# Kernel tuning notes

Hardware: AMD Instinct MI355X
Metric: run time of the kernel (lower is better)

## Reference

```python
import jax, jax.numpy as jnp
import numpy as np

B, N, D = 2, 8192, 1024
H, Dh = 16, 64
P = H * Dh
EPS = 1e-6
DECAY_BIAS_SHIFT = 2.0


def setup_inputs() -> dict:
    key = jax.random.key(0)
    ks = jax.random.split(key, 7)
    s_in = 1.0 / np.sqrt(D)
    s_out = 1.0 / np.sqrt(P)
    return {
        "x": jax.random.normal(ks[0], (B, N, D), jnp.float32),
        "Wq": jax.random.normal(ks[1], (D, P), jnp.float32) * s_in,
        "Wk": jax.random.normal(ks[2], (D, P), jnp.float32) * s_in,
        "Wv": jax.random.normal(ks[3], (D, P), jnp.float32) * s_in,
        "Wo": jax.random.normal(ks[4], (P, D), jnp.float32) * s_out,
        "Wa": jax.random.normal(ks[5], (D, H), jnp.float32) * s_in,
        "ba": jnp.zeros((H,), jnp.float32),
    }


def _elu_plus_one(x):
    return jax.nn.elu(x) + 1.0


def _ssd_scan(q, k, v, a, eps):
    # q,k,v: (B,H,N,Dh); a: (B,H,N) in (0,1)
    # Recurrence: S_t = a_t*S_{t-1} + k_t v_t^T ; z_t = a_t*z_{t-1} + k_t
    # out_t = (q_t @ S_t) / (q_t . z_t + eps)
    qT = jnp.moveaxis(q, 2, 0)  # (N,B,H,Dh)
    kT = jnp.moveaxis(k, 2, 0)
    vT = jnp.moveaxis(v, 2, 0)
    aT = jnp.moveaxis(a, 2, 0)  # (N,B,H)

    Bb, Hh, _, Dk = q.shape
    Dv = v.shape[-1]
    S0 = jnp.zeros((Bb, Hh, Dk, Dv), q.dtype)
    z0 = jnp.zeros((Bb, Hh, Dk), q.dtype)

    def step(carry, inp):
        S, z = carry
        qt, kt, vt, at = inp
        S = at[..., None, None] * S + kt[..., :, None] * vt[..., None, :]
        z = at[..., None] * z + kt
        num = jnp.einsum("bhk,bhkv->bhv", qt, S)
        den = jnp.einsum("bhk,bhk->bh", qt, z) + eps
        return (S, z), num / den[..., None]

    _, outT = jax.lax.scan(step, (S0, z0), (qT, kT, vT, aT))
    return jnp.moveaxis(outT, 0, 2)  # (B,H,N,Dv)


def reference(x, Wq, Wk, Wv, Wo, Wa, ba):
    b, n, _ = x.shape
    q = (x @ Wq).reshape(b, n, H, Dh).transpose(0, 2, 1, 3)
    k = (x @ Wk).reshape(b, n, H, Dh).transpose(0, 2, 1, 3)
    v = (x @ Wv).reshape(b, n, H, Dh).transpose(0, 2, 1, 3)
    q = _elu_plus_one(q)
    k = _elu_plus_one(k)
    a = jax.nn.sigmoid(x @ Wa + ba + DECAY_BIAS_SHIFT)  # (B,N,H)
    a = a.transpose(0, 2, 1)  # (B,H,N)
    out = _ssd_scan(q, k, v, a, EPS)  # (B,H,N,Dh)
    out = out.transpose(0, 2, 1, 3).reshape(b, n, P)
    return out @ Wo
```

## Files before the change

kernel.cpp:

```cpp
#include <hip/hip_runtime.h>
#include <stdint.h>

#define HH 16
#define DH 64
#define DD 1024
#define PP 1024
#define NNLEN 8192
#define BBATCH 2
#define MM (BBATCH*NNLEN)
#define CCHUNK 128
#define LCH 64
#define NGRP 16
#define GCH 8
#define EPSV 1e-6f

typedef unsigned short u16;
typedef __attribute__((ext_vector_type(4))) unsigned short u16x4;
typedef __attribute__((ext_vector_type(8))) unsigned short u16x8;
typedef __attribute__((ext_vector_type(8))) __bf16 bf16x8;
typedef __attribute__((ext_vector_type(4))) float f32x4;

__device__ __forceinline__ u16 f2bf(float f) {
  unsigned x = __float_as_uint(f);
  return (u16)((x + 0x7fffu + ((x >> 16) & 1u)) >> 16);
}
__device__ __forceinline__ float bf2f(u16 u) {
  return __uint_as_float(((unsigned)u) << 16);
}

__device__ __forceinline__ void gl2lds16(const void* g, void* l) {
  __builtin_amdgcn_global_load_lds(
      reinterpret_cast<__attribute__((address_space(1))) void*>(
          reinterpret_cast<uintptr_t>(g)),
      reinterpret_cast<__attribute__((address_space(3))) void*>(
          reinterpret_cast<uintptr_t>(l)),
      16, 0, 0);
}

__device__ __forceinline__ bf16x8 ldsw(const u16* base, int row, int col) {
  union { u16x8 u; bf16x8 b; } cv;
  cv.u = *(const u16x8*)&base[row * 64 + (col ^ ((row & 7) << 3))];
  return cv.b;
}

__global__ __launch_bounds__(256)
void prep_all(const float* __restrict__ x, u16* __restrict__ xb,
              const float* __restrict__ Wq, u16* __restrict__ WqT,
              const float* __restrict__ Wk, u16* __restrict__ WkT,
              const float* __restrict__ Wv, u16* __restrict__ WvT,
              const float* __restrict__ Wo, u16* __restrict__ WoT,
              const float* __restrict__ Wa, u16* __restrict__ WaT) {
  __shared__ float tile[32][33];
  const int bid = blockIdx.x;
  const int tid = threadIdx.x;
  if (bid < 8192) {
    size_t i = ((size_t)bid * 256 + tid) * 8;
    f32x4 a = *(const f32x4*)(x + i);
    f32x4 b = *(const f32x4*)(x + i + 4);
    u16x8 o;
    o[0] = f2bf(a[0]); o[1] = f2bf(a[1]); o[2] = f2bf(a[2]); o[3] = f2bf(a[3]);
    o[4] = f2bf(b[0]); o[5] = f2bf(b[1]); o[6] = f2bf(b[2]); o[7] = f2bf(b[3]);
    *(u16x8*)(xb + i) = o;
    return;
  }
  if (bid < 12288) {
    const int t = (bid - 8192) >> 10;
    const int sub = (bid - 8192) & 1023;
    const float* in = (t == 0) ? Wq : (t == 1) ? Wk : (t == 2) ? Wv : Wo;
    u16* out = (t == 0) ? WqT : (t == 1) ? WkT : (t == 2) ? WvT : WoT;
    const int bx = (sub & 31) * 32, by = (sub >> 5) * 32;
    const int tx = tid & 31, ty = tid >> 5;
    for (int i2 = ty; i2 < 32; i2 += 8)
      tile[i2][tx] = in[(size_t)(by + i2) * 1024 + bx + tx];
    __syncthreads();
    for (int i2 = ty; i2 < 32; i2 += 8)
      out[(size_t)(bx + i2) * 1024 + by + tx] = f2bf(tile[tx][i2]);
    return;
  }
  {
    int idx = (bid - 12288) * 256 + tid;
    WaT[idx] = f2bf(Wa[(idx & 1023) * 16 + (idx >> 10)]);
  }
}

__global__ __launch_bounds__(256)
void a_proj(const u16* __restrict__ xb, const u16* __restrict__ WaT,
            const float* __restrict__ ba, float* __restrict__ abuf) {
  __shared__ __align__(16) u16 As[256 * 32];
  __shared__ __align__(16) u16 Bs[16 * 32];
  const int tid = threadIdx.x;
  const int brow = blockIdx.x * 256;
  const int l = tid & 63, wid = tid >> 6;
  const int la = l & 15, kb8 = (l >> 4) * 8;
  const int sr = tid >> 2, se = (tid & 3) * 8;

  f32x4 acc[4];
#pragma unroll
  for (int mi = 0; mi < 4; ++mi) acc[mi] = (f32x4){0.f, 0.f, 0.f, 0.f};

  for (int kt = 0; kt < 32; ++kt) {
    const int k0 = kt * 32;
    __syncthreads();
#pragma unroll
    for (int i = 0; i < 4; ++i)
      gl2lds16(xb + (size_t)(brow + i * 64 + sr) * DD + k0 + se,
               &As[i * 2048 + wid * 512]);
    if (wid == 0)
      gl2lds16(WaT + (size_t)(l >> 2) * DD + k0 + (l & 3) * 8, &Bs[0]);
    __syncthreads();
    union { u16x8 u; bf16x8 b; } cvb;
    cvb.u = *(const u16x8*)&Bs[la * 32 + kb8];
#pragma unroll
    for (int mi = 0; mi < 4; ++mi) {
      union { u16x8 u; bf16x8 b; } cva;
      cva.u = *(const u16x8*)&As[(wid * 64 + mi * 16 + la) * 32 + kb8];
      acc[mi] = __builtin_amdgcn_mfma_f32_16x16x32_bf16(cva.b, cvb.b, acc[mi], 0, 0, 0);
    }
  }
  const float bav = ba[la];
#pragma unroll
  for (int mi = 0; mi < 4; ++mi)
#pragma unroll
    for (int rr = 0; rr < 4; ++rr) {
      int row = brow + wid * 64 + mi * 16 + ((l >> 4) << 2) + rr;
      float t = acc[mi][rr] + bav + 2.0f;
      abuf[(size_t)row * HH + la] = 1.f / (1.f + __expf(-t));
    }
}

template<int NCT, int ROUTE>
__global__ __launch_bounds__(512)
void gemm_db(const u16* __restrict__ A, const u16* __restrict__ Bt,
             void* __restrict__ Cout) {
  __shared__ __align__(16) u16 As[2][256 * 64];
  __shared__ __align__(16) u16 Bs[2][256 * 64];
  const int tid = threadIdx.x;
  const int nwg = gridDim.x;
  const int f = blockIdx.x;
  const int swz = (f & 7) * (nwg >> 3) + (f >> 3);
  const int brow = (swz / NCT) * 256;
  const int bcol = (swz % NCT) * 256;
  const int l = tid & 63;
  const int wid = tid >> 6;
  const int wr = wid >> 2;
  const int wc = wid & 3;
  const int la = l & 15, kb8 = (l >> 4) * 8;
  const int K = 1024;
  const int srow = l >> 3;
  const int scol = ((l & 7) * 8) ^ (srow << 3);
  const int ldso = (wid * 2) * 512;

  f32x4 acc[8][4];
#pragma unroll
  for (int i = 0; i < 8; ++i)
#pragma unroll
    for (int j = 0; j < 4; ++j) acc[i][j] = (f32x4){0.f, 0.f, 0.f, 0.f};

#pragma unroll
  for (int h = 0; h < 2; ++h)
#pragma unroll
    for (int j = 0; j < 2; ++j) {
      const int r0 = h * 128 + (wid * 2 + j) * 8 + srow;
      gl2lds16(A  + (size_t)(brow + r0) * K + scol, &As[0][h * 8192 + ldso + j * 512]);
      gl2lds16(Bt + (size_t)(bcol + r0) * K + scol, &Bs[0][h * 8192 + ldso + j * 512]);
    }
  asm volatile("s_waitcnt vmcnt(0)" ::: "memory");
  __builtin_amdgcn_s_barrier();

  const int NKT = K / 64;
  for (int kt = 0; kt < NKT; ++kt) {
    const u16* lA = As[kt & 1];
    const u16* lB = Bs[kt & 1];
    u16* nA = As[(kt + 1) & 1];
    u16* nB = Bs[(kt + 1) & 1];
    const int knext = (kt + 1) * 64;
    const bool more = (kt + 1 < NKT);

    if (more) {
#pragma unroll
      for (int h = 0; h < 2; ++h)
#pragma unroll
        for (int j = 0; j < 2; ++j) {
          const int r0 = h * 128 + (wid * 2 + j) * 8 + srow;
          gl2lds16(A  + (size_t)(brow + r0) * K + knext + scol,
                   nA + h * 8192 + ldso + j * 512);
          gl2lds16(Bt + (size_t)(bcol + r0) * K + knext + scol,
                   nB + h * 8192 + ldso + j * 512);
        }
    }

    bf16x8 af[4][2], bfr[4][2];
#pragma unroll
    for (int m2 = 0; m2 < 4; ++m2)
#pragma unroll
      for (int kk = 0; kk < 2; ++kk)
        af[m2][kk] = ldsw(lA, wr * 128 + m2 * 16 + la, kk * 32 + kb8);
#pragma unroll
    for (int n2 = 0; n2 < 4; ++n2)
#pragma unroll
      for (int kk = 0; kk < 2; ++kk)
        bfr[n2][kk] = ldsw(lB, wc * 64 + n2 * 16 + la, kk * 32 + kb8);

    __builtin_amdgcn_s_setprio(1);
#pragma unroll
    for (int m2 = 0; m2 < 4; ++m2)
#pragma unroll
      for (int n2 = 0; n2 < 4; ++n2)
#pragma unroll
        for (int kk = 0; kk < 2; ++kk)
          acc[m2][n2] = __builtin_amdgcn_mfma_f32_16x16x32_bf16(
              af[m2][kk], bfr[n2][kk], acc[m2][n2], 0, 0, 0);
    __builtin_amdgcn_s_setprio(0);

#pragma unroll
    for (int m2 = 0; m2 < 4; ++m2)
#pragma unroll
      for (int kk = 0; kk < 2; ++kk)
        af[m2][kk] = ldsw(lA, wr * 128 + 64 + m2 * 16 + la, kk * 32 + kb8);

    __builtin_amdgcn_s_setprio(1);
#pragma unroll
    for (int m2 = 0; m2 < 4; ++m2)
#pragma unroll
      for (int n2 = 0; n2 < 4; ++n2)
#pragma unroll
        for (int kk = 0; kk < 2; ++kk)
          acc[4 + m2][n2] = __builtin_amdgcn_mfma_f32_16x16x32_bf16(
              af[m2][kk], bfr[n2][kk], acc[4 + m2][n2], 0, 0, 0);
    __builtin_amdgcn_s_setprio(0);

    if (more) {
      asm volatile("s_waitcnt vmcnt(0)" ::: "memory");
      __builtin_amdgcn_s_barrier();
    }
  }

  const int wrow = wr * 128, wcol = wc * 64;
  if (ROUTE) {
    u16* base = (u16*)Cout + (size_t)(bcol >> 10) * ((size_t)MM * 1024);
    const bool act = (bcol < 2048);
#pragma unroll
    for (int mi = 0; mi < 8; ++mi)
#pragma unroll
      for (int ni = 0; ni < 4; ++ni)
#pragma unroll
        for (int rr = 0; rr < 4; ++rr) {
          int row = brow + wrow + mi * 16 + ((l >> 4) << 2) + rr;
          int c2 = (bcol & 1023) + wcol + ni * 16 + la;
          float v = acc[mi][ni][rr];
          if (act) v = v > 0.f ? v + 1.f : __expf(v);
          base[(size_t)row * 1024 + c2] = f2bf(v);
        }
  } else {
#pragma unroll
    for (int mi = 0; mi < 8; ++mi)
#pragma unroll
      for (int ni = 0; ni < 4; ++ni)
#pragma unroll
        for (int rr = 0; rr < 4; ++rr) {
          int row = brow + wrow + mi * 16 + ((l >> 4) << 2) + rr;
          int col = bcol + wcol + ni * 16 + la;
          ((float*)Cout)[(size_t)row * 1024 + col] = acc[mi][ni][rr];
        }
  }
}

__global__ __launch_bounds__(256)
void chunk_local_scan(const u16* __restrict__ kb, const u16* __restrict__ vb,
                      const float* __restrict__ abuf,
                      u16* __restrict__ Sbuf, float* __restrict__ zbuf,
                      float* __restrict__ cAbuf,
                      float* __restrict__ GAgg, float* __restrict__ zGAgg,
                      float* __restrict__ dpbuf) {
  const int g = blockIdx.x & (NGRP - 1);
  const int bh = blockIdx.x >> 4;
  const int h = bh & (HH - 1);
  const int b = bh >> 4;
  __shared__ __align__(16) u16 KT[64 * 64];
  __shared__ __align__(16) u16 VTl[64 * 64];
  __shared__ float wsh[64];
  __shared__ float dchs;
  const int tid = threadIdx.x;
  const int r = tid >> 2, e = (tid & 3) * 16;
  const int l = tid & 63, w = tid >> 6;
  const int kb8 = (l >> 4) << 3, la = l & 15;
  const int dw = 16 * w + ((l >> 4) << 2);
  const int dkz = tid >> 2, tqz = (tid & 3) * 16, swkz = (dkz & 7) << 3;

  f32x4 run[4];
#pragma unroll
  for (int ni = 0; ni < 4; ++ni) run[ni] = (f32x4){0.f, 0.f, 0.f, 0.f};
  float zrun = 0.f;
  float rp = 1.f;

  for (int i = 0; i < GCH; ++i) {
    const int c = g * GCH + i;
    const int blkc = bh * CCHUNK + c;
    const int rowbase = b * NNLEN + c * LCH;

    const u16* kp = kb + (size_t)(rowbase + r) * PP + h * DH + e;
    const u16* vp = vb + (size_t)(rowbase + r) * PP + h * DH + e;
    u16x8 k0 = *(const u16x8*)kp, k1 = *(const u16x8*)(kp + 8);
    u16x8 v0 = *(const u16x8*)vp, v1 = *(const u16x8*)(vp + 8);

    if (tid < 64) {
      float v = __logf(abuf[(size_t)(rowbase + tid) * HH + h]);
#pragma unroll
      for (int d = 1; d < 64; d <<= 1) {
        float u = __shfl_up(v, d);
        if (tid >= d) v += u;
      }
      cAbuf[(size_t)blkc * 64 + tid] = v;
      float tot = __shfl(v, 63);
      wsh[tid] = __expf(tot - v);
      if (tid == 0) dchs = __expf(tot);
    }
    __syncthreads();

    {
      const float wt = wsh[r];
#pragma unroll
      for (int j = 0; j < 8; ++j) {
        int d0 = e + j, d1 = e + 8 + j;
        KT[d0 * 64 + (r ^ ((d0 & 7) << 3))] = f2bf(bf2f(k0[j]) * wt);
        KT[d1 * 64 + (r ^ ((d1 & 7) << 3))] = f2bf(bf2f(k1[j]) * wt);
        VTl[d0 * 64 + (r ^ ((d0 & 7) << 3))] = v0[j];
        VTl[d1 * 64 + (r ^ ((d1 & 7) << 3))] = v1[j];
      }
    }
    __syncthreads();
    const float dch = dchs;

    f32x4 s[4];
#pragma unroll
    for (int ni = 0; ni < 4; ++ni) s[ni] = (f32x4){0.f, 0.f, 0.f, 0.f};
#pragma unroll
    for (int kk = 0; kk < 2; ++kk) {
      bf16x8 av = ldsw(VTl, 16 * w + la, kk * 32 + kb8);
#pragma unroll
      for (int ni = 0; ni < 4; ++ni)
        s[ni] = __builtin_amdgcn_mfma_f32_16x16x32_bf16(
            av, ldsw(KT, 16 * ni + la, kk * 32 + kb8), s[ni], 0, 0, 0);
    }

    u16* Sc = Sbuf + (size_t)blkc * 4096;
#pragma unroll
    for (int ni = 0; ni < 4; ++ni)
#pragma unroll
      for (int rr = 0; rr < 4; ++rr)
        Sc[(dw + rr) * 64 + 16 * ni + la] = f2bf(run[ni][rr]);
#pragma unroll
    for (int ni = 0; ni < 4; ++ni)
#pragma unroll
      for (int rr = 0; rr < 4; ++rr)
        run[ni][rr] = dch * run[ni][rr] + s[ni][rr];

    {
      float zp = 0.f;
#pragma unroll
      for (int i2 = 0; i2 < 16; ++i2)
        zp += bf2f(KT[dkz * 64 + ((tqz + i2) ^ swkz)]);
      zp += __shfl_xor(zp, 1);
      zp += __shfl_xor(zp, 2);
      if ((tid & 3) == 0) zbuf[(size_t)blkc * 64 + dkz] = zrun;
      zrun = dch * zrun + zp;
    }
    if (tid == 0) dpbuf[blkc] = rp;
    rp *= dch;
    __syncthreads();
  }

  float* Ga = GAgg + ((size_t)bh * NGRP + g) * 4096;
#pragma unroll
  for (int ni = 0; ni < 4; ++ni)
#pragma unroll
    for (int rr = 0; rr < 4; ++rr)
      Ga[(dw + rr) * 64 + 16 * ni + la] = run[ni][rr];
  if ((tid & 3) == 0)
    zGAgg[((size_t)bh * NGRP + g) * 64 + dkz] = zrun;
}

__global__ __launch_bounds__(1024)
void scan_top(const float* __restrict__ GAgg, u16* __restrict__ GBeg,
              float* __restrict__ zGAgg, const float* __restrict__ cAbuf) {
  const int bh = blockIdx.x;
  const size_t cb = (size_t)bh * CCHUNK;
  __shared__ float Dsh[NGRP];
  if (threadIdx.x < NGRP) {
    float s = 0.f;
#pragma unroll
    for (int i = 0; i < GCH; ++i)
      s += cAbuf[(cb + threadIdx.x * GCH + i) * 64 + 63];
    Dsh[threadIdx.x] = __expf(s);
  }
  __syncthreads();
  const int elem = threadIdx.x * 4;
  const float* base = GAgg + (size_t)bh * NGRP * 4096;
  u16* gb = GBeg + (size_t)bh * NGRP * 4096;
  f32x4 run = (f32x4){0.f, 0.f, 0.f, 0.f};
  f32x4 cur = *(const f32x4*)&base[elem];
#pragma unroll
  for (int gg = 0; gg < NGRP; ++gg) {
    f32x4 nxt;
    if (gg + 1 < NGRP) nxt = *(const f32x4*)&base[(gg + 1) * 4096 + elem];
    u16x4 o;
#pragma unroll
    for (int jj = 0; jj < 4; ++jj) o[jj] = f2bf(run[jj]);
    *(u16x4*)&gb[gg * 4096 + elem] = o;
    const float D = Dsh[gg];
#pragma unroll
    for (int jj = 0; jj < 4; ++jj) run[jj] = D * run[jj] + cur[jj];
    cur = nxt;
  }
  if (threadIdx.x < 64) {
    float* zb = zGAgg + (size_t)bh * NGRP * 64;
    float zr = 0.f;
#pragma unroll
    for (int gg = 0; gg < NGRP; ++gg) {
      float a = zb[gg * 64 + threadIdx.x];
      zb[gg * 64 + threadIdx.x] = zr;
      zr = Dsh[gg] * zr + a;
    }
  }
}

__global__ __launch_bounds__(256)
void chunk_out(u16* __restrict__ qb, const u16* __restrict__ kb,
               const u16* __restrict__ vb, const u16* __restrict__ Sbuf,
               const float* __restrict__ zbuf, const float* __restrict__ cAbuf,
               const u16* __restrict__ GBeg, const float* __restrict__ zGAgg,
               const float* __restrict__ dpbuf) {
  const int blk = blockIdx.x;
  const int c = blk & (CCHUNK - 1);
  const int h = (blk >> 7) & (HH - 1);
  const int b = blk >> 11;
  const int bh = blk >> 7;
  const int g = c >> 3;
  const int rowbase = b * NNLEN + c * LCH;

  __shared__ __align__(16) u16 Qs[64 * 64];
  __shared__ __align__(16) u16 Ke[64 * 64];
  __shared__ __align__(16) u16 VT[64 * 64];
  __shared__ __align__(16) u16 STs[64 * 64];
  __shared__ float cAsh[64], zsh[64], denP[64], qzs[64];

  const int tid = threadIdx.x;
  const int r = tid >> 2, e = (tid & 3) * 16;
  const float dp = dpbuf[blk];

  const u16* qp = qb + (size_t)(rowbase + r) * PP + h * DH + e;
  const u16* kp = kb + (size_t)(rowbase + r) * PP + h * DH + e;
  const u16* vp = vb + (size_t)(rowbase + r) * PP + h * DH + e;
  u16x8 q0 = *(const u16x8*)qp, q1 = *(const u16x8*)(qp + 8);
  u16x8 k0 = *(const u16x8*)kp, k1 = *(const u16x8*)(kp + 8);
  u16x8 v0 = *(const u16x8*)vp, v1 = *(const u16x8*)(vp + 8);
  const u16* sp = Sbuf + (size_t)blk * 4096 + r * 64 + e;
  u16x8 p0 = *(const u16x8*)sp, p1 = *(const u16x8*)(sp + 8);
  const u16* gp = GBeg + ((size_t)bh * NGRP + g) * 4096 + r * 64 + e;
  u16x8 gb0 = *(const u16x8*)gp, gb1 = *(const u16x8*)(gp + 8);
  if (tid < 64) {
    cAsh[tid] = cAbuf[(size_t)blk * 64 + tid];
    zsh[tid] = zbuf[(size_t)blk * 64 + tid]
             + dp * zGAgg[((size_t)bh * NGRP + g) * 64 + tid];
  }
  __syncthreads();

  {
    const float c0c = cAsh[31];
    const int sw = (r & 7) << 3;
    const float qsc = __expf(cAsh[r] - c0c);
    const float ksc = __expf(c0c - cAsh[r]);
    const float ssc = __expf(c0c);
    u16x8 t0, t1, u0, u1, w0, w1;
#pragma unroll
    for (int j = 0; j < 8; ++j) {
      t0[j] = f2bf(bf2f(q0[j]) * qsc);
      t1[j] = f2bf(bf2f(q1[j]) * qsc);
      u0[j] = f2bf(bf2f(k0[j]) * ksc);
      u1[j] = f2bf(bf2f(k1[j]) * ksc);
    }
#pragma unroll
    for (int j = 0; j < 8; ++j) {
      w0[j] = f2bf((bf2f(p0[j]) + dp * bf2f(gb0[j])) * ssc);
      w1[j] = f2bf((bf2f(p1[j]) + dp * bf2f(gb1[j])) * ssc);
    }
    *(u16x8*)&Qs[r * 64 + (e ^ sw)] = t0;
    *(u16x8*)&Qs[r * 64 + ((e + 8) ^ sw)] = t1;
    *(u16x8*)&Ke[r * 64 + (e ^ sw)] = u0;
    *(u16x8*)&Ke[r * 64 + ((e + 8) ^ sw)] = u1;
    *(u16x8*)&STs[r * 64 + (e ^ sw)] = w0;
    *(u16x8*)&STs[r * 64 + ((e + 8) ^ sw)] = w1;
#pragma unroll
    for (int j = 0; j < 8; ++j) {
      int d0 = e + j, d1 = e + 8 + j;
      VT[d0 * 64 + (r ^ ((d0 & 7) << 3))] = v0[j];
      VT[d1 * 64 + (r ^ ((d1 & 7) << 3))] = v1[j];
    }
    if (tid < 64) zsh[tid] *= ssc;
  }
  __syncthreads();

  const int l = tid & 63, w = tid >> 6;
  const int kb8 = (l >> 4) << 3, la = l & 15;

  bf16x8 aq[2];
  f32x4 p[4];
#pragma unroll
  for (int ni = 0; ni < 4; ++ni) p[ni] = (f32x4){0.f, 0.f, 0.f, 0.f};
#pragma unroll
  for (int kk = 0; kk < 2; ++kk) {
    aq[kk] = ldsw(Qs, 16 * w + la, kk * 32 + kb8);
#pragma unroll
    for (int ni = 0; ni < 4; ++ni)
      p[ni] = __builtin_amdgcn_mfma_f32_16x16x32_bf16(
          aq[kk], ldsw(Ke, 16 * ni + la, kk * 32 + kb8), p[ni], 0, 0, 0);
  }

  const int tw = 16 * w + ((l >> 4) << 2);
  float rsum[4] = {0.f, 0.f, 0.f, 0.f};
#pragma unroll
  for (int ni = 0; ni < 4; ++ni)
#pragma unroll
    for (int rr = 0; rr < 4; ++rr) {
      int s = 16 * ni + la, t = tw + rr;
      float v = (s <= t) ? p[ni][rr] : 0.f;
      p[ni][rr] = v;
      rsum[rr] += v;
    }
#pragma unroll
  for (int d = 1; d < 16; d <<= 1)
#pragma unroll
    for (int rr = 0; rr < 4; ++rr) rsum[rr] += __shfl_xor(rsum[rr], d);
  if (la == 0)
#pragma unroll
    for (int rr = 0; rr < 4; ++rr) denP[tw + rr] = rsum[rr];

  {
    float qzp = 0.f;
#pragma unroll
    for (int kk = 0; kk < 2; ++kk)
#pragma unroll
      for (int j = 0; j < 8; ++j) {
        union { bf16x8 b; u16x8 u; } cv; cv.b = aq[kk];
        qzp += bf2f(cv.u[j]) * zsh[kk * 32 + kb8 + j];
      }
    qzp += __shfl_xor(qzp, 16);
    qzp += __shfl_xor(qzp, 32);
    if (l < 16) qzs[16 * w + la] = qzp;
  }
  __syncthreads();

#pragma unroll
  for (int ni = 0; ni < 4; ++ni)
#pragma unroll
    for (int rr = 0; rr < 4; ++rr) {
      int t = tw + rr, s = 16 * ni + la;
      Ke[t * 64 + (s ^ ((t & 7) << 3))] = f2bf(p[ni][rr]);
    }
  __syncthreads();

  f32x4 o[4];
#pragma unroll
  for (int ni = 0; ni < 4; ++ni) o[ni] = (f32x4){0.f, 0.f, 0.f, 0.f};
#pragma unroll
  for (int kk = 0; kk < 2; ++kk) {
    bf16x8 ap = ldsw(Ke, 16 * w + la, kk * 32 + kb8);
#pragma unroll
    for (int ni = 0; ni < 4; ++ni)
      o[ni] = __builtin_amdgcn_mfma_f32_16x16x32_bf16(
          ap, ldsw(VT, 16 * ni + la, kk * 32 + kb8), o[ni], 0, 0, 0);
  }
#pragma unroll
  for (int kk = 0; kk < 2; ++kk)
#pragma unroll
    for (int ni = 0; ni < 4; ++ni)
      o[ni] = __builtin_amdgcn_mfma_f32_16x16x32_bf16(
          aq[kk], ldsw(STs, 16 * ni + la, kk * 32 + kb8), o[ni], 0, 0, 0);

  float dn[4];
#pragma unroll
  for (int rr = 0; rr < 4; ++rr) dn[rr] = qzs[tw + rr] + denP[tw + rr] + EPSV;
#pragma unroll
  for (int ni = 0; ni < 4; ++ni)
#pragma unroll
    for (int rr = 0; rr < 4; ++rr) {
      int t = tw + rr, dv = 16 * ni + la;
      qb[(size_t)(rowbase + t) * PP + h * DH + dv] = f2bf(o[ni][rr] / dn[rr]);
    }
}

extern "C" void kernel_launch(void* const* d_in, const int* in_sizes, int n_in,
                              void* d_out, int out_size, void* d_ws, size_t ws_size,
                              hipStream_t stream) {
  const float* x  = (const float*)d_in[0];
  const float* Wq = (const float*)d_in[1];
  const float* Wk = (const float*)d_in[2];
  const float* Wv = (const float*)d_in[3];
  const float* Wo = (const float*)d_in[4];
  const float* Wa = (const float*)d_in[5];
  const float* ba = (const float*)d_in[6];

  char* ws = (char*)d_ws;
  size_t off = 0;
  auto carve = [&](size_t bytes) {
    void* p = ws + off;
    off += (bytes + 255) & ~(size_t)255;
    return p;
  };
  u16* xb   = (u16*)carve((size_t)MM * DD * 2);
  u16* WqT  = (u16*)carve((size_t)PP * DD * 2);
  u16* WkT  = (u16*)carve((size_t)PP * DD * 2);
  u16* WvT  = (u16*)carve((size_t)PP * DD * 2);
  u16* WoT  = (u16*)carve((size_t)DD * PP * 2);
  u16* WaT  = (u16*)carve((size_t)HH * DD * 2);
  u16* qb   = (u16*)carve((size_t)MM * PP * 2);
  u16* kb   = (u16*)carve((size_t)MM * PP * 2);
  u16* vb   = (u16*)carve((size_t)MM * PP * 2);
  float* abuf  = (float*)carve((size_t)MM * HH * 4);
  u16*  Sbuf   = (u16*)carve((size_t)BBATCH * HH * CCHUNK * 4096 * 2);
  float* zbuf  = (float*)carve((size_t)BBATCH * HH * CCHUNK * 64 * 4);
  float* cAbuf = (float*)carve((size_t)BBATCH * HH * CCHUNK * 64 * 4);
  float* GAgg  = (float*)carve((size_t)BBATCH * HH * NGRP * 4096 * 4);
  u16*  GBeg   = (u16*)carve((size_t)BBATCH * HH * NGRP * 4096 * 2);
  float* zGAgg = (float*)carve((size_t)BBATCH * HH * NGRP * 64 * 4);
  float* dpbuf = (float*)carve((size_t)BBATCH * HH * CCHUNK * 4);

  prep_all<<<12352, 256, 0, stream>>>(x, xb, Wq, WqT, Wk, WkT, Wv, WvT,
                                      Wo, WoT, Wa, WaT);
  a_proj<<<MM / 256, 256, 0, stream>>>(xb, WaT, ba, abuf);

  gemm_db<12, 1><<<(MM / 256) * 12, 512, 0, stream>>>(xb, WqT, qb);

  chunk_local_scan<<<BBATCH * HH * NGRP, 256, 0, stream>>>(
      kb, vb, abuf, Sbuf, zbuf, cAbuf, GAgg, zGAgg, dpbuf);
  scan_top<<<BBATCH * HH, 1024, 0, stream>>>(GAgg, GBeg, zGAgg, cAbuf);
  chunk_out<<<BBATCH * HH * CCHUNK, 256, 0, stream>>>(qb, kb, vb, Sbuf, zbuf, cAbuf,
                                                      GBeg, zGAgg, dpbuf);

  gemm_db<4, 0><<<(MM / 256) * 4, 512, 0, stream>>>(qb, WoT, (float*)d_out);
}
```

Baseline: 253.7 us.

## Shrink GEMM tiles to 256x128xK32 and hoist decay prefix sums in chunk scan

The GEMM kernel drops from 256x256 tiles with a K-step of 64 to 256x128 tiles with a K-step of 32. This cuts LDS use and accumulator registers so four workgroups can be resident per CU, and it doubles the grid size. A new swizzle layout for the 32-wide LDS rows comes with it. The chunk-local scan now computes all eight chunks' log-decay prefix sums up front in parallel across warps, prefetches the next chunk's k/v into registers, and drops one barrier per iteration. The trade-off is more K iterations and barriers in the GEMM, plus less reuse per tile.

```diff
diff --git a/kernel.cpp b/kernel.cpp
--- a/kernel.cpp
+++ b/kernel.cpp
@@ -40,6 +40,12 @@
 __device__ __forceinline__ bf16x8 ldsw(const u16* base, int row, int col) {
   union { u16x8 u; bf16x8 b; } cv;
   cv.u = *(const u16x8*)&base[row * 64 + (col ^ ((row & 7) << 3))];
+  return cv.b;
+}
+
+__device__ __forceinline__ bf16x8 ldsw32(const u16* base, int row, int col) {
+  union { u16x8 u; bf16x8 b; } cv;
+  cv.u = *(const u16x8*)&base[row * 32 + (col ^ (((row >> 1) & 3) << 3))];
   return cv.b;
 }
 
@@ -129,104 +135,75 @@
 }
 
 template<int NCT, int ROUTE>
-__global__ __launch_bounds__(512)
-void gemm_db(const u16* __restrict__ A, const u16* __restrict__ Bt,
+__global__ __launch_bounds__(512, 4)
+void gemm_tb(const u16* __restrict__ A, const u16* __restrict__ Bt,
              void* __restrict__ Cout) {
-  __shared__ __align__(16) u16 As[2][256 * 64];
-  __shared__ __align__(16) u16 Bs[2][256 * 64];
+  __shared__ __align__(16) u16 As[2][256 * 32];
+  __shared__ __align__(16) u16 Bs[2][128 * 32];
   const int tid = threadIdx.x;
   const int nwg = gridDim.x;
   const int f = blockIdx.x;
   const int swz = (f & 7) * (nwg >> 3) + (f >> 3);
   const int brow = (swz / NCT) * 256;
-  const int bcol = (swz % NCT) * 256;
+  const int bcol = (swz % NCT) * 128;
   const int l = tid & 63;
   const int wid = tid >> 6;
-  const int wr = wid >> 2;
-  const int wc = wid & 3;
+  const int wrow = (wid >> 1) * 64;
+  const int wcol = (wid & 1) * 64;
   const int la = l & 15, kb8 = (l >> 4) * 8;
   const int K = 1024;
-  const int srow = l >> 3;
-  const int scol = ((l & 7) * 8) ^ (srow << 3);
-  const int ldso = (wid * 2) * 512;
-
-  f32x4 acc[8][4];
-#pragma unroll
-  for (int i = 0; i < 8; ++i)
+  const int srow = l >> 2;
+  const int scol = (((l & 3) ^ ((l >> 3) & 3)) << 3);
+
+  f32x4 acc[4][4];
+#pragma unroll
+  for (int i = 0; i < 4; ++i)
 #pragma unroll
     for (int j = 0; j < 4; ++j) acc[i][j] = (f32x4){0.f, 0.f, 0.f, 0.f};
 
 #pragma unroll
-  for (int h = 0; h < 2; ++h)
-#pragma unroll
-    for (int j = 0; j < 2; ++j) {
-      const int r0 = h * 128 + (wid * 2 + j) * 8 + srow;
-      gl2lds16(A  + (size_t)(brow + r0) * K + scol, &As[0][h * 8192 + ldso + j * 512]);
-      gl2lds16(Bt + (size_t)(bcol + r0) * K + scol, &Bs[0][h * 8192 + ldso + j * 512]);
-    }
+  for (int j = 0; j < 2; ++j) {
+    const int r0 = (wid * 2 + j) * 16 + srow;
+    gl2lds16(A + (size_t)(brow + r0) * K + scol, &As[0][(wid * 2 + j) * 512]);
+  }
+  gl2lds16(Bt + (size_t)(bcol + wid * 16 + srow) * K + scol, &Bs[0][wid * 512]);
   asm volatile("s_waitcnt vmcnt(0)" ::: "memory");
   __builtin_amdgcn_s_barrier();
 
-  const int NKT = K / 64;
+  const int NKT = K / 32;
   for (int kt = 0; kt < NKT; ++kt) {
     const u16* lA = As[kt & 1];
     const u16* lB = Bs[kt & 1];
     u16* nA = As[(kt + 1) & 1];
     u16* nB = Bs[(kt + 1) & 1];
-    const int knext = (kt + 1) * 64;
+    const int knext = (kt + 1) * 32;
     const bool more = (kt + 1 < NKT);
 
     if (more) {
 #pragma unroll
-      for (int h = 0; h < 2; ++h)
-#pragma unroll
-        for (int j = 0; j < 2; ++j) {
-          const int r0 = h * 128 + (wid * 2 + j) * 8 + srow;
-          gl2lds16(A  + (size_t)(brow + r0) * K + knext + scol,
-                   nA + h * 8192 + ldso + j * 512);
-          gl2lds16(Bt + (size_t)(bcol + r0) * K + knext + scol,
-                   nB + h * 8192 + ldso + j * 512);
-        }
-    }
-
-    bf16x8 af[4][2], bfr[4][2];
-#pragma unroll
-    for (int m2 = 0; m2 < 4; ++m2)
-#pragma unroll
-      for (int kk = 0; kk < 2; ++kk)
-        af[m2][kk] = ldsw(lA, wr * 128 + m2 * 16 + la, kk * 32 + kb8);
+      for (int j = 0; j < 2; ++j) {
+        const int r0 = (wid * 2 + j) * 16 + srow;
+        gl2lds16(A + (size_t)(brow + r0) * K + knext + scol,
+                 nA + (wid * 2 + j) * 512);
+      }
+      gl2lds16(Bt + (size_t)(bcol + wid * 16 + srow) * K + knext + scol,
+               nB + wid * 512);
+    }
+
+    bf16x8 bfr[4];
 #pragma unroll
     for (int n2 = 0; n2 < 4; ++n2)
-#pragma unroll
-      for (int kk = 0; kk < 2; ++kk)
-        bfr[n2][kk] = ldsw(lB, wc * 64 + n2 * 16 + la, kk * 32 + kb8);
+      bfr[n2] = ldsw32(lB, wcol + n2 * 16 + la, kb8);
 
     __builtin_amdgcn_s_setprio(1);
 #pragma unroll
-    for (int m2 = 0; m2 < 4; ++m2)
+    for (int m2 = 0; m2 < 4; ++m2) {
+      bf16x8 afm = ldsw32(lA, wrow + m2 * 16 + la, kb8);
 #pragma unroll
       for (int n2 = 0; n2 < 4; ++n2)
-#pragma unroll
-        for (int kk = 0; kk < 2; ++kk)
-          acc[m2][n2] = __builtin_amdgcn_mfma_f32_16x16x32_bf16(
-              af[m2][kk], bfr[n2][kk], acc[m2][n2], 0, 0, 0);
-    __builtin_amdgcn_s_setprio(0);
-
-#pragma unroll
-    for (int m2 = 0; m2 < 4; ++m2)
-#pragma unroll
-      for (int kk = 0; kk < 2; ++kk)
-        af[m2][kk] = ldsw(lA, wr * 128 + 64 + m2 * 16 + la, kk * 32 + kb8);
-
-    __builtin_amdgcn_s_setprio(1);
-#pragma unroll
-    for (int m2 = 0; m2 < 4; ++m2)
-#pragma unroll
-      for (int n2 = 0; n2 < 4; ++n2)
-#pragma unroll
-        for (int kk = 0; kk < 2; ++kk)
-          acc[4 + m2][n2] = __builtin_amdgcn_mfma_f32_16x16x32_bf16(
-              af[m2][kk], bfr[n2][kk], acc[4 + m2][n2], 0, 0, 0);
+        acc[m2][n2] = __builtin_amdgcn_mfma_f32_16x16x32_bf16(
+            afm, bfr[n2], acc[m2][n2], 0, 0, 0);
+    }
     __builtin_amdgcn_s_setprio(0);
 
     if (more) {
@@ -235,12 +212,11 @@
     }
   }
 
-  const int wrow = wr * 128, wcol = wc * 64;
   if (ROUTE) {
     u16* base = (u16*)Cout + (size_t)(bcol >> 10) * ((size_t)MM * 1024);
     const bool act = (bcol < 2048);
 #pragma unroll
-    for (int mi = 0; mi < 8; ++mi)
+    for (int mi = 0; mi < 4; ++mi)
 #pragma unroll
       for (int ni = 0; ni < 4; ++ni)
 #pragma unroll
@@ -253,7 +229,7 @@
         }
   } else {
 #pragma unroll
-    for (int mi = 0; mi < 8; ++mi)
+    for (int mi = 0; mi < 4; ++mi)
 #pragma unroll
       for (int ni = 0; ni < 4; ++ni)
 #pragma unroll
@@ -278,47 +254,58 @@
   const int b = bh >> 4;
   __shared__ __align__(16) u16 KT[64 * 64];
   __shared__ __align__(16) u16 VTl[64 * 64];
-  __shared__ float wsh[64];
-  __shared__ float dchs;
+  __shared__ float wshA[GCH][64];
+  __shared__ float dchA[GCH];
   const int tid = threadIdx.x;
   const int r = tid >> 2, e = (tid & 3) * 16;
   const int l = tid & 63, w = tid >> 6;
   const int kb8 = (l >> 4) << 3, la = l & 15;
   const int dw = 16 * w + ((l >> 4) << 2);
   const int dkz = tid >> 2, tqz = (tid & 3) * 16, swkz = (dkz & 7) << 3;
+  const int c0 = g * GCH;
+  const int rowbase0 = b * NNLEN + c0 * LCH;
+
+#pragma unroll
+  for (int ii = 0; ii < 2; ++ii) {
+    const int i = w * 2 + ii;
+    const int blkc = bh * CCHUNK + c0 + i;
+    float v = __logf(abuf[(size_t)(rowbase0 + i * LCH + l) * HH + h]);
+#pragma unroll
+    for (int d = 1; d < 64; d <<= 1) {
+      float u = __shfl_up(v, d);
+      if (l >= d) v += u;
+    }
+    cAbuf[(size_t)blkc * 64 + l] = v;
+    float tot = __shfl(v, 63);
+    wshA[i][l] = __expf(tot - v);
+    if (l == 0) dchA[i] = __expf(tot);
+  }
+  __syncthreads();
+  if (tid == 0) {
+    float rp = 1.f;
+#pragma unroll
+    for (int i = 0; i < GCH; ++i) {
+      dpbuf[bh * CCHUNK + c0 + i] = rp;
+      rp *= dchA[i];
+    }
+  }
 
   f32x4 run[4];
 #pragma unroll
   for (int ni = 0; ni < 4; ++ni) run[ni] = (f32x4){0.f, 0.f, 0.f, 0.f};
   float zrun = 0.f;
-  float rp = 1.f;
+
+  const u16* kp = kb + (size_t)(rowbase0 + r) * PP + h * DH + e;
+  const u16* vp = vb + (size_t)(rowbase0 + r) * PP + h * DH + e;
+  u16x8 k0 = *(const u16x8*)kp, k1 = *(const u16x8*)(kp + 8);
+  u16x8 v0 = *(const u16x8*)vp, v1 = *(const u16x8*)(vp + 8);
 
   for (int i = 0; i < GCH; ++i) {
-    const int c = g * GCH + i;
-    const int blkc = bh * CCHUNK + c;
-    const int rowbase = b * NNLEN + c * LCH;
-
-    const u16* kp = kb + (size_t)(rowbase + r) * PP + h * DH + e;
-    const u16* vp = vb + (size_t)(rowbase + r) * PP + h * DH + e;
-    u16x8 k0 = *(const u16x8*)kp, k1 = *(const u16x8*)(kp + 8);
-    u16x8 v0 = *(const u16x8*)vp, v1 = *(const u16x8*)(vp + 8);
-
-    if (tid < 64) {
-      float v = __logf(abuf[(size_t)(rowbase + tid) * HH + h]);
-#pragma unroll
-      for (int d = 1; d < 64; d <<= 1) {
-        float u = __shfl_up(v, d);
-        if (tid >= d) v += u;
-      }
-      cAbuf[(size_t)blkc * 64 + tid] = v;
-      float tot = __shfl(v, 63);
-      wsh[tid] = __expf(tot - v);
-      if (tid == 0) dchs = __expf(tot);
-    }
-    __syncthreads();
+    const int blkc = bh * CCHUNK + c0 + i;
+    if (i) __syncthreads();
 
     {
-      const float wt = wsh[r];
+      const float wt = wshA[i][r];
 #pragma unroll
       for (int j = 0; j < 8; ++j) {
         int d0 = e + j, d1 = e + 8 + j;
@@ -329,8 +316,16 @@
       }
     }
     __syncthreads();
-    const float dch = dchs;
-
+
+    if (i + 1 < GCH) {
+      const int rb = rowbase0 + (i + 1) * LCH;
+      kp = kb + (size_t)(rb + r) * PP + h * DH + e;
+      vp = vb + (size_t)(rb + r) * PP + h * DH + e;
+      k0 = *(const u16x8*)kp; k1 = *(const u16x8*)(kp + 8);
+      v0 = *(const u16x8*)vp; v1 = *(const u16x8*)(vp + 8);
+    }
+
+    const float dch = dchA[i];
     f32x4 s[4];
 #pragma unroll
     for (int ni = 0; ni < 4; ++ni) s[ni] = (f32x4){0.f, 0.f, 0.f, 0.f};
@@ -365,9 +360,6 @@
       if ((tid & 3) == 0) zbuf[(size_t)blkc * 64 + dkz] = zrun;
       zrun = dch * zrun + zp;
     }
-    if (tid == 0) dpbuf[blkc] = rp;
-    rp *= dch;
-    __syncthreads();
   }
 
   float* Ga = GAgg + ((size_t)bh * NGRP + g) * 4096;
@@ -629,7 +621,7 @@
                                       Wo, WoT, Wa, WaT);
   a_proj<<<MM / 256, 256, 0, stream>>>(xb, WaT, ba, abuf);
 
-  gemm_db<12, 1><<<(MM / 256) * 12, 512, 0, stream>>>(xb, WqT, qb);
+  gemm_tb<24, 1><<<(MM / 256) * 24, 512, 0, stream>>>(xb, WqT, qb);
 
   chunk_local_scan<<<BBATCH * HH * NGRP, 256, 0, stream>>>(
       kb, vb, abuf, Sbuf, zbuf, cAbuf, GAgg, zGAgg, dpbuf);
@@ -637,5 +629,5 @@
   chunk_out<<<BBATCH * HH * CCHUNK, 256, 0, stream>>>(qb, kb, vb, Sbuf, zbuf, cAbuf,
                                                       GBeg, zGAgg, dpbuf);
 
-  gemm_db<4, 0><<<(MM / 256) * 4, 512, 0, stream>>>(qb, WoT, (float*)d_out);
-}
+  gemm_tb<8, 0><<<(MM / 256) * 8, 512, 0, stream>>>(qb, WoT, (float*)d_out);
+}
```

Measured after the change: 264.7 us. 1.04x slower.

## Fuse decay projection into QKV GEMM launch and prefetch chunk-scan loads

Applied to the files above, without the earlier changes.

Removes the separate a_proj launch by appending its blocks to the QKV GEMM grid, so the decay sigmoid projection runs as extra workgroups of the same kernel. The GEMM tile mapping becomes an XCD-aware scheme that gives each XCD a contiguous row range. In chunk_local_scan, all eight per-chunk decay prefix scans are computed up front, and the next chunk's k/v loads are prefetched into registers during the current chunk's MFMA work, which also drops one barrier per iteration. This adds register pressure and shares a launch between heterogeneous blocks.

```diff
diff --git a/kernel.cpp b/kernel.cpp
--- a/kernel.cpp
+++ b/kernel.cpp
@@ -83,69 +83,65 @@
   }
 }
 
-__global__ __launch_bounds__(256)
-void a_proj(const u16* __restrict__ xb, const u16* __restrict__ WaT,
-            const float* __restrict__ ba, float* __restrict__ abuf) {
-  __shared__ __align__(16) u16 As[256 * 32];
-  __shared__ __align__(16) u16 Bs[16 * 32];
-  const int tid = threadIdx.x;
-  const int brow = blockIdx.x * 256;
-  const int l = tid & 63, wid = tid >> 6;
-  const int la = l & 15, kb8 = (l >> 4) * 8;
-  const int sr = tid >> 2, se = (tid & 3) * 8;
-
-  f32x4 acc[4];
-#pragma unroll
-  for (int mi = 0; mi < 4; ++mi) acc[mi] = (f32x4){0.f, 0.f, 0.f, 0.f};
-
-  for (int kt = 0; kt < 32; ++kt) {
-    const int k0 = kt * 32;
-    __syncthreads();
-#pragma unroll
-    for (int i = 0; i < 4; ++i)
-      gl2lds16(xb + (size_t)(brow + i * 64 + sr) * DD + k0 + se,
-               &As[i * 2048 + wid * 512]);
-    if (wid == 0)
-      gl2lds16(WaT + (size_t)(l >> 2) * DD + k0 + (l & 3) * 8, &Bs[0]);
-    __syncthreads();
-    union { u16x8 u; bf16x8 b; } cvb;
-    cvb.u = *(const u16x8*)&Bs[la * 32 + kb8];
-#pragma unroll
-    for (int mi = 0; mi < 4; ++mi) {
-      union { u16x8 u; bf16x8 b; } cva;
-      cva.u = *(const u16x8*)&As[(wid * 64 + mi * 16 + la) * 32 + kb8];
-      acc[mi] = __builtin_amdgcn_mfma_f32_16x16x32_bf16(cva.b, cvb.b, acc[mi], 0, 0, 0);
-    }
-  }
-  const float bav = ba[la];
-#pragma unroll
-  for (int mi = 0; mi < 4; ++mi)
-#pragma unroll
-    for (int rr = 0; rr < 4; ++rr) {
-      int row = brow + wid * 64 + mi * 16 + ((l >> 4) << 2) + rr;
-      float t = acc[mi][rr] + bav + 2.0f;
-      abuf[(size_t)row * HH + la] = 1.f / (1.f + __expf(-t));
-    }
-}
-
-template<int NCT, int ROUTE>
+template<int NCT, int NGT, int ROUTE>
 __global__ __launch_bounds__(512)
 void gemm_db(const u16* __restrict__ A, const u16* __restrict__ Bt,
-             void* __restrict__ Cout) {
+             void* __restrict__ Cout, const u16* __restrict__ WaT,
+             const float* __restrict__ ba, float* __restrict__ abuf) {
   __shared__ __align__(16) u16 As[2][256 * 64];
   __shared__ __align__(16) u16 Bs[2][256 * 64];
   const int tid = threadIdx.x;
-  const int nwg = gridDim.x;
   const int f = blockIdx.x;
-  const int swz = (f & 7) * (nwg >> 3) + (f >> 3);
-  const int brow = (swz / NCT) * 256;
-  const int bcol = (swz % NCT) * 256;
   const int l = tid & 63;
   const int wid = tid >> 6;
+  const int la = l & 15, kb8 = (l >> 4) * 8;
+  const int K = 1024;
+
+  if (ROUTE && f >= NGT) {
+    const int brow2 = (f - NGT) * 256;
+    const int sr = tid >> 2, se = (tid & 3) * 8;
+    u16* As0 = As[0];
+    u16* Bs0 = Bs[0];
+    f32x4 acc2[2];
+    acc2[0] = (f32x4){0.f, 0.f, 0.f, 0.f};
+    acc2[1] = (f32x4){0.f, 0.f, 0.f, 0.f};
+    for (int kt = 0; kt < 32; ++kt) {
+      const int k0 = kt * 32;
+      __syncthreads();
+      gl2lds16(A + (size_t)(brow2 + sr) * DD + k0 + se, &As0[wid * 512]);
+      gl2lds16(A + (size_t)(brow2 + 128 + sr) * DD + k0 + se,
+               &As0[4096 + wid * 512]);
+      if (wid == 0)
+        gl2lds16(WaT + (size_t)(l >> 2) * DD + k0 + (l & 3) * 8, &Bs0[0]);
+      __syncthreads();
+      union { u16x8 u; bf16x8 b; } cvb;
+      cvb.u = *(const u16x8*)&Bs0[la * 32 + kb8];
+#pragma unroll
+      for (int mi = 0; mi < 2; ++mi) {
+        union { u16x8 u; bf16x8 b; } cva;
+        cva.u = *(const u16x8*)&As0[(wid * 32 + mi * 16 + la) * 32 + kb8];
+        acc2[mi] = __builtin_amdgcn_mfma_f32_16x16x32_bf16(cva.b, cvb.b, acc2[mi], 0, 0, 0);
+      }
+    }
+    const float bav = ba[la];
+#pragma unroll
+    for (int mi = 0; mi < 2; ++mi)
+#pragma unroll
+      for (int rr = 0; rr < 4; ++rr) {
+        int row = brow2 + wid * 32 + mi * 16 + ((l >> 4) << 2) + rr;
+        float t = acc2[mi][rr] + bav + 2.0f;
+        abuf[(size_t)row * HH + la] = 1.f / (1.f + __expf(-t));
+      }
+    return;
+  }
+
+  const int C = NGT >> 3;
+  const int R = C / NCT;
+  const int xcd = f & 7, loc = f >> 3;
+  const int brow = (xcd * R + loc % R) * 256;
+  const int bcol = (loc / R) * 256;
   const int wr = wid >> 2;
   const int wc = wid & 3;
-  const int la = l & 15, kb8 = (l >> 4) * 8;
-  const int K = 1024;
   const int srow = l >> 3;
   const int scol = ((l & 7) * 8) ^ (srow << 3);
   const int ldso = (wid * 2) * 512;
@@ -278,47 +274,58 @@
   const int b = bh >> 4;
   __shared__ __align__(16) u16 KT[64 * 64];
   __shared__ __align__(16) u16 VTl[64 * 64];
-  __shared__ float wsh[64];
-  __shared__ float dchs;
+  __shared__ float wshA[GCH][64];
+  __shared__ float dchA[GCH];
   const int tid = threadIdx.x;
   const int r = tid >> 2, e = (tid & 3) * 16;
   const int l = tid & 63, w = tid >> 6;
   const int kb8 = (l >> 4) << 3, la = l & 15;
   const int dw = 16 * w + ((l >> 4) << 2);
   const int dkz = tid >> 2, tqz = (tid & 3) * 16, swkz = (dkz & 7) << 3;
+  const int c0 = g * GCH;
+  const int rowbase0 = b * NNLEN + c0 * LCH;
+
+#pragma unroll
+  for (int ii = 0; ii < 2; ++ii) {
+    const int i = w * 2 + ii;
+    const int blkc = bh * CCHUNK + c0 + i;
+    float v = __logf(abuf[(size_t)(rowbase0 + i * LCH + l) * HH + h]);
+#pragma unroll
+    for (int d = 1; d < 64; d <<= 1) {
+      float u = __shfl_up(v, d);
+      if (l >= d) v += u;
+    }
+    cAbuf[(size_t)blkc * 64 + l] = v;
+    float tot = __shfl(v, 63);
+    wshA[i][l] = __expf(tot - v);
+    if (l == 0) dchA[i] = __expf(tot);
+  }
+  __syncthreads();
+  if (tid == 0) {
+    float rp = 1.f;
+#pragma unroll
+    for (int i = 0; i < GCH; ++i) {
+      dpbuf[bh * CCHUNK + c0 + i] = rp;
+      rp *= dchA[i];
+    }
+  }
 
   f32x4 run[4];
 #pragma unroll
   for (int ni = 0; ni < 4; ++ni) run[ni] = (f32x4){0.f, 0.f, 0.f, 0.f};
   float zrun = 0.f;
-  float rp = 1.f;
+
+  const u16* kp = kb + (size_t)(rowbase0 + r) * PP + h * DH + e;
+  const u16* vp = vb + (size_t)(rowbase0 + r) * PP + h * DH + e;
+  u16x8 k0 = *(const u16x8*)kp, k1 = *(const u16x8*)(kp + 8);
+  u16x8 v0 = *(const u16x8*)vp, v1 = *(const u16x8*)(vp + 8);
 
   for (int i = 0; i < GCH; ++i) {
-    const int c = g * GCH + i;
-    const int blkc = bh * CCHUNK + c;
-    const int rowbase = b * NNLEN + c * LCH;
-
-    const u16* kp = kb + (size_t)(rowbase + r) * PP + h * DH + e;
-    const u16* vp = vb + (size_t)(rowbase + r) * PP + h * DH + e;
-    u16x8 k0 = *(const u16x8*)kp, k1 = *(const u16x8*)(kp + 8);
-    u16x8 v0 = *(const u16x8*)vp, v1 = *(const u16x8*)(vp + 8);
-
-    if (tid < 64) {
-      float v = __logf(abuf[(size_t)(rowbase + tid) * HH + h]);
-#pragma unroll
-      for (int d = 1; d < 64; d <<= 1) {
-        float u = __shfl_up(v, d);
-        if (tid >= d) v += u;
-      }
-      cAbuf[(size_t)blkc * 64 + tid] = v;
-      float tot = __shfl(v, 63);
-      wsh[tid] = __expf(tot - v);
-      if (tid == 0) dchs = __expf(tot);
-    }
-    __syncthreads();
+    const int blkc = bh * CCHUNK + c0 + i;
+    if (i) __syncthreads();
 
     {
-      const float wt = wsh[r];
+      const float wt = wshA[i][r];
 #pragma unroll
       for (int j = 0; j < 8; ++j) {
         int d0 = e + j, d1 = e + 8 + j;
@@ -329,8 +336,16 @@
       }
     }
     __syncthreads();
-    const float dch = dchs;
-
+
+    if (i + 1 < GCH) {
+      const int rb = rowbase0 + (i + 1) * LCH;
+      kp = kb + (size_t)(rb + r) * PP + h * DH + e;
+      vp = vb + (size_t)(rb + r) * PP + h * DH + e;
+      k0 = *(const u16x8*)kp; k1 = *(const u16x8*)(kp + 8);
+      v0 = *(const u16x8*)vp; v1 = *(const u16x8*)(vp + 8);
+    }
+
+    const float dch = dchA[i];
     f32x4 s[4];
 #pragma unroll
     for (int ni = 0; ni < 4; ++ni) s[ni] = (f32x4){0.f, 0.f, 0.f, 0.f};
@@ -365,9 +380,6 @@
       if ((tid & 3) == 0) zbuf[(size_t)blkc * 64 + dkz] = zrun;
       zrun = dch * zrun + zp;
     }
-    if (tid == 0) dpbuf[blkc] = rp;
-    rp *= dch;
-    __syncthreads();
   }
 
   float* Ga = GAgg + ((size_t)bh * NGRP + g) * 4096;
@@ -627,9 +639,9 @@
 
   prep_all<<<12352, 256, 0, stream>>>(x, xb, Wq, WqT, Wk, WkT, Wv, WvT,
                                       Wo, WoT, Wa, WaT);
-  a_proj<<<MM / 256, 256, 0, stream>>>(xb, WaT, ba, abuf);
-
-  gemm_db<12, 1><<<(MM / 256) * 12, 512, 0, stream>>>(xb, WqT, qb);
+
+  gemm_db<12, 768, 1><<<768 + MM / 256, 512, 0, stream>>>(
+      xb, WqT, qb, WaT, ba, abuf);
 
   chunk_local_scan<<<BBATCH * HH * NGRP, 256, 0, stream>>>(
       kb, vb, abuf, Sbuf, zbuf, cAbuf, GAgg, zGAgg, dpbuf);
@@ -637,5 +649,6 @@
   chunk_out<<<BBATCH * HH * CCHUNK, 256, 0, stream>>>(qb, kb, vb, Sbuf, zbuf, cAbuf,
                                                       GBeg, zGAgg, dpbuf);
 
-  gemm_db<4, 0><<<(MM / 256) * 4, 512, 0, stream>>>(qb, WoT, (float*)d_out);
-}
+  gemm_db<4, 256, 0><<<256, 512, 0, stream>>>(qb, WoT, (float*)d_out,
+                                              nullptr, nullptr, nullptr);
+}
```

Measured after the change: 246.4 us. 1.03x faster.
